# Optimization experiments

Hardware: AMD Instinct MI355X
Metric: run time of the kernel (lower is better)

The kernel has to match this reference:

```python
import jax, jax.numpy as jnp
import numpy as np

WS = 8          # window_size
NH = 8          # num_heads
DIM = 512
EPS = 1e-5


def _layernorm(x, gamma, beta):
    mu = jnp.mean(x, axis=-1, keepdims=True)
    var = jnp.mean(jnp.square(x - mu), axis=-1, keepdims=True)
    return (x - mu) * jax.lax.rsqrt(var + EPS) * gamma + beta


def setup_inputs() -> dict:
    key = jax.random.key(0)
    ks = jax.random.split(key, 16)
    B, C, H, W = 8, DIM, 128, 128
    s = 0.02
    return {
        "x": jax.random.normal(ks[0], (B, C, H, W), jnp.float32),
        "gamma1": jnp.ones((C,), jnp.float32),
        "beta1": jnp.zeros((C,), jnp.float32),
        "gamma2": jnp.ones((C,), jnp.float32),
        "beta2": jnp.zeros((C,), jnp.float32),
        "w_qkv": jax.random.normal(ks[1], (C, 3 * C), jnp.float32) * s,
        "b_qkv": jnp.zeros((3 * C,), jnp.float32),
        "w_out": jax.random.normal(ks[2], (C, C), jnp.float32) * s,
        "b_out": jnp.zeros((C,), jnp.float32),
        "w1": jax.random.normal(ks[3], (C, 4 * C), jnp.float32) * s,
        "b1": jnp.zeros((4 * C,), jnp.float32),
        "w2": jax.random.normal(ks[4], (4 * C, C), jnp.float32) * s,
        "b2": jnp.zeros((C,), jnp.float32),
    }


def reference(x, gamma1, beta1, gamma2, beta2, w_qkv, b_qkv, w_out, b_out, w1, b1, w2, b2):
    B, C, H, W = x.shape
    hd = C // NH          # head_dim = 64
    L = WS * WS           # tokens per window = 64
    N = (H // WS) * (W // WS)

    # window_partition: (B,C,H,W) -> (B,N,C,ws,ws)
    xw = x.reshape(B, C, H // WS, WS, W // WS, WS)
    xw = xw.transpose(0, 1, 2, 4, 3, 5).reshape(B, C, N, WS, WS).transpose(0, 2, 1, 3, 4)
    # spatial_flatten -> (B,N,L,C)
    t = xw.reshape(B, N, C, L).transpose(0, 1, 3, 2)

    # --- attention (non-transposed path) ---
    xn = _layernorm(t, gamma1, beta1)
    qkv = jnp.einsum('bnlc,cd->bnld', xn, w_qkv) + b_qkv
    qkv = qkv.reshape(B, N, L, 3, NH, hd).transpose(3, 0, 1, 4, 2, 5)  # (3,B,N,H,L,hd)
    q, k, v = qkv[0], qkv[1], qkv[2]
    # note: module scales by 1/head_dim on BOTH q and k -> 1/hd^2 total
    scores = jnp.einsum('bnhld,bnhmd->bnhlm', q, k) / (hd * hd)
    attn = jax.nn.softmax(scores, axis=-1)
    o = jnp.einsum('bnhlm,bnhmd->bnhld', attn, v)
    o = o.transpose(0, 1, 3, 2, 4).reshape(B, N, L, C)
    o = jnp.einsum('bnlc,cd->bnld', o, w_out) + b_out
    t = t + o

    # --- MLP ---
    xn2 = _layernorm(t, gamma2, beta2)
    h = jax.nn.gelu(jnp.einsum('bnlc,cd->bnld', xn2, w1) + b1, approximate=False)
    t = t + jnp.einsum('bnld,dc->bnlc', h, w2) + b2

    # spatial_unflatten + window_unpartition -> (B,C,H,W)
    y = t.transpose(0, 1, 3, 2).reshape(B, N, C, WS, WS).transpose(0, 2, 1, 3, 4)
    y = y.reshape(B, C, H // WS, W // WS, WS, WS).transpose(0, 1, 2, 4, 3, 5).reshape(B, C, H, W)
    return y
```

## Files before the change

### kernel.cpp

```cpp
#include <hip/hip_runtime.h>
#include <cstdint>
#include <cstddef>


typedef unsigned short u16;
typedef unsigned int u32;
typedef __attribute__((ext_vector_type(4))) float f32x4;
typedef __attribute__((ext_vector_type(8))) short bf16x8;

#define DEVINL __device__ __forceinline__

DEVINL float bf2f(u16 u){ union { u32 i; float f; } v; v.i = ((u32)u) << 16; return v.f; }
DEVINL u16 f2bf(float f){
  union { float f; u32 i; } v; v.f = f;
  u32 u = v.i;
  u32 r = (u + 0x7fffu + ((u >> 16) & 1u)) >> 16;
  return (u16)r;
}

DEVINL void gload16(u16* lds, const void* g){
  __builtin_amdgcn_global_load_lds(
      (__attribute__((address_space(1))) u32*)(g),
      (__attribute__((address_space(3))) u32*)(lds), 16, 0, 0);
}

__global__ __launch_bounds__(256) void wt_kernel(const float* __restrict__ in,
                                                 u16* __restrict__ out, int K, int N)
{
  __shared__ float tile[64][65];
  int tiles_n = N >> 6;
  int tk = blockIdx.x / tiles_n, tn = blockIdx.x % tiles_n;
  int k0 = tk * 64, n0 = tn * 64;
  int lane = threadIdx.x & 63, wr = threadIdx.x >> 6;
#pragma unroll
  for (int i = 0; i < 16; i++){
    int r = wr * 16 + i;
    tile[r][lane] = in[(size_t)(k0 + r) * N + n0 + lane];
  }
  __syncthreads();
#pragma unroll
  for (int i = 0; i < 16; i++){
    int r = wr * 16 + i;
    out[(size_t)(n0 + r) * K + k0 + lane] = f2bf(tile[lane][r]);
  }
}

template<int MODE>
__global__ __launch_bounds__(256) void ln_kernel(
    const float* __restrict__ x, const u16* __restrict__ o2,
    const float* __restrict__ gamma, const float* __restrict__ beta,
    u16* __restrict__ out)
{
  __shared__ u16 sm[512 * 64];
  int wg = blockIdx.x;
  int b = wg >> 8, n = wg & 255, wy = n >> 4, wx = n & 15;
  int t = threadIdx.x, l = t & 63, wv = t >> 6;
  int yy = l >> 3, xx = l & 7;
  size_t xbase = ((size_t)b * 512) * 16384 + (size_t)(wy * 8 + yy) * 128 + wx * 8 + xx;

#pragma unroll 4
  for (int i = 0; i < 128; i++){
    int c = wv * 128 + i;
    float v = x[xbase + (size_t)c * 16384];
    sm[c * 64 + (l ^ ((2 * (c >> 3)) & 63))] = f2bf(v);
  }
  __syncthreads();

  size_t gbase = (size_t)wg * 64;
  int lane = l;
  int c0 = lane * 8;
  int fs = (2 * lane) & 63;
  float g8[8], b8[8];
#pragma unroll
  for (int j = 0; j < 8; j++){ g8[j] = gamma[c0 + j]; b8[j] = beta[c0 + j]; }

  for (int it = 0; it < 16; it++){
    int tok = wv * 16 + it;
    int lidx = tok ^ fs;
    u16 oarr[8];
    if (MODE == 1){
      uint4 ov = *(const uint4*)&o2[(gbase + tok) * 512 + c0];
      *(uint4*)oarr = ov;
    }
    float tv[8]; float sum = 0.f, sq = 0.f;
#pragma unroll
    for (int j = 0; j < 8; j++){
      float v = bf2f(sm[(c0 + j) * 64 + lidx]);
      if (MODE == 1) v += bf2f(oarr[j]);
      tv[j] = v; sum += v; sq += v * v;
    }
#pragma unroll
    for (int d = 1; d < 64; d <<= 1){
      sum += __shfl_xor(sum, d, 64);
      sq  += __shfl_xor(sq, d, 64);
    }
    float mu = sum * (1.0f / 512.0f);
    float var = sq * (1.0f / 512.0f) - mu * mu;
    float rs = rsqrtf(var + 1e-5f);
    u16 r8[8];
#pragma unroll
    for (int j = 0; j < 8; j++) r8[j] = f2bf((tv[j] - mu) * rs * g8[j] + b8[j]);
    *(uint4*)&out[(gbase + tok) * 512 + c0] = *(uint4*)r8;
  }
}

template<int EPI>
__global__ __launch_bounds__(256) void gemm_kernel(
    const u16* __restrict__ A, const u16* __restrict__ BT,
    const float* __restrict__ bias, const u16* __restrict__ ADD,
    u16* __restrict__ Cout, int N, int K)
{
  __shared__ u16 smem[16384];
  const int nbn = N >> 7;
  int nwg = gridDim.x;
  int bid = blockIdx.x;
  int wgid = (bid & 7) * (nwg >> 3) + (bid >> 3);
  int bm = wgid / nbn, bn = wgid % nbn;
  size_t m0 = (size_t)bm * 128; int n0 = bn * 128;
  int lane = threadIdx.x & 63, wv = threadIdx.x >> 6;
  int wr = wv >> 1, wc = wv & 1;

  f32x4 zero4 = {0.f, 0.f, 0.f, 0.f};
  f32x4 acc[4][4];
#pragma unroll
  for (int i = 0; i < 4; i++)
#pragma unroll
    for (int j = 0; j < 4; j++) acc[i][j] = zero4;

  int srow = wv * 16 + (lane >> 2);
  int scol = (((lane & 3) ^ ((srow >> 1) & 3)) * 8);
  const u16* Abase = A + m0 * (size_t)K;
  const u16* Bbase = BT + (size_t)n0 * K;

  auto STAGE = [&](int buf, int kt){
    u16* as = &smem[buf * 8192];
    u16* bs = as + 4096;
    gload16(as + wv * 512,        Abase + (size_t)srow * K + kt + scol);
    gload16(as + 2048 + wv * 512, Abase + (size_t)(srow + 64) * K + kt + scol);
    gload16(bs + wv * 512,        Bbase + (size_t)srow * K + kt + scol);
    gload16(bs + 2048 + wv * 512, Bbase + (size_t)(srow + 64) * K + kt + scol);
  };

  STAGE(0, 0);
  __syncthreads();

  int nsteps = K >> 5;
  int cur = 0;
  int kslot = lane >> 4;
  for (int t = 0; t < nsteps; ++t){
    if (t + 1 < nsteps) STAGE(cur ^ 1, (t + 1) << 5);
    const u16* as = &smem[cur * 8192];
    const u16* bs = as + 4096;
    bf16x8 af[4], bfr[4];
#pragma unroll
    for (int mt = 0; mt < 4; mt++){
      int row = wr * 64 + mt * 16 + (lane & 15);
      af[mt] = *(const bf16x8*)&as[row * 32 + ((kslot ^ ((row >> 1) & 3)) * 8)];
    }
#pragma unroll
    for (int nt = 0; nt < 4; nt++){
      int row = wc * 64 + nt * 16 + (lane & 15);
      bfr[nt] = *(const bf16x8*)&bs[row * 32 + ((kslot ^ ((row >> 1) & 3)) * 8)];
    }
#pragma unroll
    for (int mt = 0; mt < 4; mt++)
#pragma unroll
      for (int nt = 0; nt < 4; nt++)
        acc[mt][nt] = __builtin_amdgcn_mfma_f32_16x16x32_bf16(af[mt], bfr[nt], acc[mt][nt], 0, 0, 0);
    __syncthreads();
    cur ^= 1;
  }

#pragma unroll
  for (int nt = 0; nt < 4; nt++){
    int cc = wc * 64 + nt * 16 + (lane & 15);
    float bv = bias[n0 + cc];
#pragma unroll
    for (int mt = 0; mt < 4; mt++){
      int r0 = wr * 64 + mt * 16 + ((lane >> 4) * 4);
#pragma unroll
      for (int reg = 0; reg < 4; reg++){
        int rr = r0 + reg;
        float v = acc[mt][nt][reg] + bv;
        if (EPI == 1){
          float h2 = v * v;
          float z = -1.5957691216057308f * (v + 0.044715f * v * h2);
          float e = __expf(z);
          v = v * __builtin_amdgcn_rcpf(1.0f + e);
        }
        smem[rr * 128 + (cc ^ ((rr & 7) << 3))] = f2bf(v);
      }
    }
  }
  __syncthreads();

  int tr = threadIdx.x >> 2;
  int tc = threadIdx.x & 3;
#pragma unroll
  for (int i = 0; i < 2; i++){
    int r = i * 64 + tr;
    size_t gro = (m0 + r) * (size_t)N + n0;
#pragma unroll
    for (int j = 0; j < 4; j++){
      int cw = tc * 8 + j * 32;
      uint4 d = *(const uint4*)&smem[r * 128 + (cw ^ ((r & 7) << 3))];
      if (EPI == 2){
        uint4 av = *(const uint4*)&ADD[gro + cw];
        u16 de[8], ae[8];
        *(uint4*)de = d; *(uint4*)ae = av;
#pragma unroll
        for (int k = 0; k < 8; k++) de[k] = f2bf(bf2f(de[k]) + bf2f(ae[k]));
        d = *(uint4*)de;
      }
      *(uint4*)&Cout[gro + cw] = d;
    }
  }
}

__global__ __launch_bounds__(64) void attn_kernel(const u16* __restrict__ QKV,
                                                  u16* __restrict__ O)
{
  __shared__ u16 qs[4096], ks2[4096], vs[4096], ps[4096];
  int blk = blockIdx.x;
  int wg = blk >> 3, h = blk & 7;
  size_t g0 = (size_t)wg * 64;
  int lane = threadIdx.x;
  int lr = lane >> 3, lch = lane & 7;

#pragma unroll
  for (int it = 0; it < 8; it++){
    int r = it * 8 + lr;
    int sc = lch ^ (r & 7);
    {
      uint4 d = *(const uint4*)&QKV[(g0 + r) * 1536 + h * 64 + lch * 8];
      *(uint4*)&qs[r * 64 + sc * 8] = d;
    }
    {
      uint4 d = *(const uint4*)&QKV[(g0 + r) * 1536 + 512 + h * 64 + lch * 8];
      *(uint4*)&ks2[r * 64 + sc * 8] = d;
    }
    {
      uint4 d = *(const uint4*)&QKV[(g0 + r) * 1536 + 1024 + h * 64 + lch * 8];
      u16 e[8]; *(uint4*)e = d;
      int m = r;
#pragma unroll
      for (int j = 0; j < 8; j++){
        int dd = lch * 8 + j;
        int off = dd * 64 + ((((m * 2) ^ ((dd & 7) << 4))) >> 1);
        vs[off] = e[j];
      }
    }
  }
  __syncthreads();

  f32x4 zero4 = {0.f, 0.f, 0.f, 0.f};
  f32x4 s[4][4];
#pragma unroll
  for (int i = 0; i < 4; i++)
#pragma unroll
    for (int j = 0; j < 4; j++) s[i][j] = zero4;

#pragma unroll
  for (int ks = 0; ks < 2; ks++){
    bf16x8 aq[4], bk[4];
#pragma unroll
    for (int mt = 0; mt < 4; mt++){
      int r = mt * 16 + (lane & 15);
      int cb = (ks * 64 + (lane >> 4) * 16) ^ ((r & 7) << 4);
      aq[mt] = *(const bf16x8*)&qs[r * 64 + (cb >> 1)];
    }
#pragma unroll
    for (int nt = 0; nt < 4; nt++){
      int r = nt * 16 + (lane & 15);
      int cb = (ks * 64 + (lane >> 4) * 16) ^ ((r & 7) << 4);
      bk[nt] = *(const bf16x8*)&ks2[r * 64 + (cb >> 1)];
    }
#pragma unroll
    for (int mt = 0; mt < 4; mt++)
#pragma unroll
      for (int nt = 0; nt < 4; nt++)
        s[mt][nt] = __builtin_amdgcn_mfma_f32_16x16x32_bf16(aq[mt], bk[nt], s[mt][nt], 0, 0, 0);
  }

  const float scl = 1.0f / 4096.0f;
#pragma unroll
  for (int mt = 0; mt < 4; mt++){
#pragma unroll
    for (int reg = 0; reg < 4; reg++){
      float mx = -1e30f;
#pragma unroll
      for (int nt = 0; nt < 4; nt++){
        float v = s[mt][nt][reg] * scl; s[mt][nt][reg] = v; mx = fmaxf(mx, v);
      }
#pragma unroll
      for (int d = 1; d < 16; d <<= 1) mx = fmaxf(mx, __shfl_xor(mx, d, 64));
      float sum = 0.f;
#pragma unroll
      for (int nt = 0; nt < 4; nt++){
        float e = __expf(s[mt][nt][reg] - mx); s[mt][nt][reg] = e; sum += e;
      }
#pragma unroll
      for (int d = 1; d < 16; d <<= 1) sum += __shfl_xor(sum, d, 64);
      float inv = 1.0f / sum;
#pragma unroll
      for (int nt = 0; nt < 4; nt++) s[mt][nt][reg] *= inv;
    }
  }

#pragma unroll
  for (int mt = 0; mt < 4; mt++)
#pragma unroll
    for (int reg = 0; reg < 4; reg++){
      int r = mt * 16 + ((lane >> 4) * 4) + reg;
#pragma unroll
      for (int nt = 0; nt < 4; nt++){
        int c = nt * 16 + (lane & 15);
        ps[r * 64 + ((((c * 2) ^ ((r & 7) << 4))) >> 1)] = f2bf(s[mt][nt][reg]);
      }
    }
  __syncthreads();

  f32x4 o[4][4];
#pragma unroll
  for (int i = 0; i < 4; i++)
#pragma unroll
    for (int j = 0; j < 4; j++) o[i][j] = zero4;

#pragma unroll
  for (int ks = 0; ks < 2; ks++){
    bf16x8 ap[4], bv[4];
#pragma unroll
    for (int mt = 0; mt < 4; mt++){
      int r = mt * 16 + (lane & 15);
      int cb = (ks * 64 + (lane >> 4) * 16) ^ ((r & 7) << 4);
      ap[mt] = *(const bf16x8*)&ps[r * 64 + (cb >> 1)];
    }
#pragma unroll
    for (int nt = 0; nt < 4; nt++){
      int dd = nt * 16 + (lane & 15);
      int cb = (ks * 64 + (lane >> 4) * 16) ^ ((dd & 7) << 4);
      bv[nt] = *(const bf16x8*)&vs[dd * 64 + (cb >> 1)];
    }
#pragma unroll
    for (int mt = 0; mt < 4; mt++)
#pragma unroll
      for (int nt = 0; nt < 4; nt++)
        o[mt][nt] = __builtin_amdgcn_mfma_f32_16x16x32_bf16(ap[mt], bv[nt], o[mt][nt], 0, 0, 0);
  }

#pragma unroll
  for (int mt = 0; mt < 4; mt++)
#pragma unroll
    for (int reg = 0; reg < 4; reg++){
      size_t l = mt * 16 + ((lane >> 4) * 4) + reg;
#pragma unroll
      for (int nt = 0; nt < 4; nt++){
        int dd = nt * 16 + (lane & 15);
        O[(g0 + l) * 512 + h * 64 + dd] = f2bf(o[mt][nt][reg]);
      }
    }
}

__global__ __launch_bounds__(256) void scatter_kernel(
    const float* __restrict__ x, const u16* __restrict__ ms, float* __restrict__ y)
{
  __shared__ u16 sm[512 * 64];
  int wg = blockIdx.x;
  int b = wg >> 8, n = wg & 255, wy = n >> 4, wx = n & 15;
  int t = threadIdx.x, lane = t & 63, wv = t >> 6;
  size_t gbase = (size_t)wg * 64;
  int c0 = lane * 8, fs = (2 * lane) & 63;

  for (int it = 0; it < 16; it++){
    int tok = wv * 16 + it;
    uint4 d = *(const uint4*)&ms[(gbase + tok) * 512 + c0];
    u16 e[8]; *(uint4*)e = d;
    int lidx = tok ^ fs;
#pragma unroll
    for (int j = 0; j < 8; j++) sm[(c0 + j) * 64 + lidx] = e[j];
  }
  __syncthreads();

  int l = lane; int yy = l >> 3, xx = l & 7;
  size_t xbase = ((size_t)b * 512) * 16384 + (size_t)(wy * 8 + yy) * 128 + wx * 8 + xx;
#pragma unroll 4
  for (int i = 0; i < 128; i++){
    int c = wv * 128 + i;
    size_t a = xbase + (size_t)c * 16384;
    y[a] = x[a] + bf2f(sm[c * 64 + (l ^ ((2 * (c >> 3)) & 63))]);
  }
}

extern "C" void kernel_launch(void* const* d_in, const int* in_sizes, int n_in,
                              void* d_out, int out_size, void* d_ws, size_t ws_size,
                              hipStream_t stream)
{
  (void)in_sizes; (void)n_in; (void)out_size; (void)ws_size;
  const float* x      = (const float*)d_in[0];
  const float* gamma1 = (const float*)d_in[1];
  const float* beta1  = (const float*)d_in[2];
  const float* gamma2 = (const float*)d_in[3];
  const float* beta2  = (const float*)d_in[4];
  const float* w_qkv  = (const float*)d_in[5];
  const float* b_qkv  = (const float*)d_in[6];
  const float* w_out  = (const float*)d_in[7];
  const float* b_out  = (const float*)d_in[8];
  const float* w1     = (const float*)d_in[9];
  const float* b1     = (const float*)d_in[10];
  const float* w2     = (const float*)d_in[11];
  const float* b2     = (const float*)d_in[12];
  float* y = (float*)d_out;

  char* ws = (char*)d_ws;
  u16* WqkvT = (u16*)(ws + 0);
  u16* WoutT = (u16*)(ws + 1572864);
  u16* W1T   = (u16*)(ws + 2097152);
  u16* W2T   = (u16*)(ws + 4194304);
  u16* XN    = (u16*)(ws + 6291456);
  u16* O2    = (u16*)(ws + 140509184);
  u16* Obuf  = (u16*)(ws + 274726912);
  u16* QKV   = (u16*)(ws + 408944640);
  u16* Hbuf  = QKV;
  u16* MS    = Obuf;
  const int M = 131072;

  wt_kernel<<<8 * 24, 256, 0, stream>>>(w_qkv, WqkvT, 512, 1536);
  wt_kernel<<<8 * 8,  256, 0, stream>>>(w_out, WoutT, 512, 512);
  wt_kernel<<<8 * 32, 256, 0, stream>>>(w1, W1T, 512, 2048);
  wt_kernel<<<32 * 8, 256, 0, stream>>>(w2, W2T, 2048, 512);

  ln_kernel<0><<<2048, 256, 0, stream>>>(x, nullptr, gamma1, beta1, XN);
  gemm_kernel<0><<<(M / 128) * (1536 / 128), 256, 0, stream>>>(XN, WqkvT, b_qkv, nullptr, QKV, 1536, 512);
  attn_kernel<<<16384, 64, 0, stream>>>(QKV, Obuf);
  gemm_kernel<0><<<(M / 128) * (512 / 128), 256, 0, stream>>>(Obuf, WoutT, b_out, nullptr, O2, 512, 512);
  ln_kernel<1><<<2048, 256, 0, stream>>>(x, O2, gamma2, beta2, XN);
  gemm_kernel<1><<<(M / 128) * (2048 / 128), 256, 0, stream>>>(XN, W1T, b1, nullptr, Hbuf, 2048, 512);
  gemm_kernel<2><<<(M / 128) * (512 / 128), 256, 0, stream>>>(Hbuf, W2T, b2, O2, MS, 512, 2048);
  scatter_kernel<<<2048, 256, 0, stream>>>(x, MS, y);
}
```

Before: 2.457 ms.

## Use 256x256 GEMM tiles with 8 waves and a 4-slot LDS pipeline

Replaces the 128x128, 4-wave GEMM with a 256x256 tile computed by 8 waves. It uses a four-slot LDS ring with three tiles of prefetch and explicit vmcnt waits in place of the double buffer plus __syncthreads, and raises wave priority around the MFMA block. The larger tile raises arithmetic intensity and cuts global traffic per FLOP, while the deeper prefetch hides load latency. In exchange it uses 128KB of LDS and more accumulator registers per block, which limits occupancy. The N=512 GEMMs also launch far fewer blocks, which risks tail imbalance.

```diff
diff --git a/kernel.cpp b/kernel.cpp
--- a/kernel.cpp
+++ b/kernel.cpp
@@ -105,115 +105,115 @@
 }
 
 template<int EPI>
-__global__ __launch_bounds__(256) void gemm_kernel(
+__global__ __launch_bounds__(512, 2) void gemm256_kernel(
     const u16* __restrict__ A, const u16* __restrict__ BT,
     const float* __restrict__ bias, const u16* __restrict__ ADD,
     u16* __restrict__ Cout, int N, int K)
 {
-  __shared__ u16 smem[16384];
-  const int nbn = N >> 7;
+  __shared__ u16 smem[65536];
+  const int nbn = N >> 8;
   int nwg = gridDim.x;
   int bid = blockIdx.x;
   int wgid = (bid & 7) * (nwg >> 3) + (bid >> 3);
   int bm = wgid / nbn, bn = wgid % nbn;
-  size_t m0 = (size_t)bm * 128; int n0 = bn * 128;
-  int lane = threadIdx.x & 63, wv = threadIdx.x >> 6;
-  int wr = wv >> 1, wc = wv & 1;
+  size_t m0 = (size_t)bm * 256; int n0 = bn * 256;
+  int tid = threadIdx.x;
+  int lane = tid & 63, w = tid >> 6;
+  int wr = w >> 2, wc = w & 3;
 
   f32x4 zero4 = {0.f, 0.f, 0.f, 0.f};
-  f32x4 acc[4][4];
-#pragma unroll
-  for (int i = 0; i < 4; i++)
+  f32x4 acc[8][4];
+#pragma unroll
+  for (int i = 0; i < 8; i++)
 #pragma unroll
     for (int j = 0; j < 4; j++) acc[i][j] = zero4;
 
-  int srow = wv * 16 + (lane >> 2);
-  int scol = (((lane & 3) ^ ((srow >> 1) & 3)) * 8);
+  int sr = tid >> 2;
+  int scol = (((tid & 3) ^ ((sr >> 1) & 3)) * 8);
   const u16* Abase = A + m0 * (size_t)K;
   const u16* Bbase = BT + (size_t)n0 * K;
 
-  auto STAGE = [&](int buf, int kt){
-    u16* as = &smem[buf * 8192];
-    u16* bs = as + 4096;
-    gload16(as + wv * 512,        Abase + (size_t)srow * K + kt + scol);
-    gload16(as + 2048 + wv * 512, Abase + (size_t)(srow + 64) * K + kt + scol);
-    gload16(bs + wv * 512,        Bbase + (size_t)srow * K + kt + scol);
-    gload16(bs + 2048 + wv * 512, Bbase + (size_t)(srow + 64) * K + kt + scol);
+  auto STAGE = [&](int slot, int kt){
+    u16* s = &smem[slot * 16384];
+    gload16(s + w * 512,          Abase + (size_t)sr * K + kt + scol);
+    gload16(s + 4096 + w * 512,   Abase + (size_t)(sr + 128) * K + kt + scol);
+    gload16(s + 8192 + w * 512,   Bbase + (size_t)sr * K + kt + scol);
+    gload16(s + 12288 + w * 512,  Bbase + (size_t)(sr + 128) * K + kt + scol);
   };
 
-  STAGE(0, 0);
-  __syncthreads();
-
-  int nsteps = K >> 5;
-  int cur = 0;
+  int nk = K >> 5;
+  STAGE(0, 0); STAGE(1, 32); STAGE(2, 64);
+
   int kslot = lane >> 4;
-  for (int t = 0; t < nsteps; ++t){
-    if (t + 1 < nsteps) STAGE(cur ^ 1, (t + 1) << 5);
-    const u16* as = &smem[cur * 8192];
-    const u16* bs = as + 4096;
-    bf16x8 af[4], bfr[4];
-#pragma unroll
-    for (int mt = 0; mt < 4; mt++){
-      int row = wr * 64 + mt * 16 + (lane & 15);
-      af[mt] = *(const bf16x8*)&as[row * 32 + ((kslot ^ ((row >> 1) & 3)) * 8)];
-    }
-#pragma unroll
-    for (int nt = 0; nt < 4; nt++){
-      int row = wc * 64 + nt * 16 + (lane & 15);
-      bfr[nt] = *(const bf16x8*)&bs[row * 32 + ((kslot ^ ((row >> 1) & 3)) * 8)];
-    }
-#pragma unroll
-    for (int mt = 0; mt < 4; mt++)
-#pragma unroll
-      for (int nt = 0; nt < 4; nt++)
-        acc[mt][nt] = __builtin_amdgcn_mfma_f32_16x16x32_bf16(af[mt], bfr[nt], acc[mt][nt], 0, 0, 0);
-    __syncthreads();
-    cur ^= 1;
-  }
-
-#pragma unroll
-  for (int nt = 0; nt < 4; nt++){
-    int cc = wc * 64 + nt * 16 + (lane & 15);
+  for (int t = 0; t < nk; ++t){
+    if (t < nk - 2)      asm volatile("s_waitcnt vmcnt(8)" ::: "memory");
+    else if (t == nk - 2) asm volatile("s_waitcnt vmcnt(4)" ::: "memory");
+    else                  asm volatile("s_waitcnt vmcnt(0)" ::: "memory");
+    __builtin_amdgcn_s_barrier();
+    if (t + 3 < nk) STAGE((t + 3) & 3, (t + 3) << 5);
+
+    const u16* as = &smem[(t & 3) * 16384];
+    const u16* bs = as + 8192;
+    bf16x8 af[8], bf[4];
+#pragma unroll
+    for (int m = 0; m < 8; m++){
+      int row = wr * 128 + m * 16 + (lane & 15);
+      af[m] = *(const bf16x8*)&as[row * 32 + ((kslot ^ ((row >> 1) & 3)) * 8)];
+    }
+#pragma unroll
+    for (int n = 0; n < 4; n++){
+      int row = wc * 64 + n * 16 + (lane & 15);
+      bf[n] = *(const bf16x8*)&bs[row * 32 + ((kslot ^ ((row >> 1) & 3)) * 8)];
+    }
+    __builtin_amdgcn_s_setprio(1);
+#pragma unroll
+    for (int m = 0; m < 8; m++)
+#pragma unroll
+      for (int n = 0; n < 4; n++)
+        acc[m][n] = __builtin_amdgcn_mfma_f32_16x16x32_bf16(af[m], bf[n], acc[m][n], 0, 0, 0);
+    __builtin_amdgcn_s_setprio(0);
+  }
+
+  __syncthreads();
+
+#pragma unroll
+  for (int n = 0; n < 4; n++){
+    int cc = wc * 64 + n * 16 + (lane & 15);
     float bv = bias[n0 + cc];
 #pragma unroll
-    for (int mt = 0; mt < 4; mt++){
-      int r0 = wr * 64 + mt * 16 + ((lane >> 4) * 4);
+    for (int m = 0; m < 8; m++){
+      int r0 = wr * 128 + m * 16 + ((lane >> 4) * 4);
 #pragma unroll
       for (int reg = 0; reg < 4; reg++){
         int rr = r0 + reg;
-        float v = acc[mt][nt][reg] + bv;
+        float v = acc[m][n][reg] + bv;
         if (EPI == 1){
           float h2 = v * v;
           float z = -1.5957691216057308f * (v + 0.044715f * v * h2);
           float e = __expf(z);
           v = v * __builtin_amdgcn_rcpf(1.0f + e);
         }
-        smem[rr * 128 + (cc ^ ((rr & 7) << 3))] = f2bf(v);
-      }
-    }
-  }
-  __syncthreads();
-
-  int tr = threadIdx.x >> 2;
-  int tc = threadIdx.x & 3;
-#pragma unroll
-  for (int i = 0; i < 2; i++){
-    int r = i * 64 + tr;
-    size_t gro = (m0 + r) * (size_t)N + n0;
-#pragma unroll
-    for (int j = 0; j < 4; j++){
-      int cw = tc * 8 + j * 32;
-      uint4 d = *(const uint4*)&smem[r * 128 + (cw ^ ((r & 7) << 3))];
-      if (EPI == 2){
-        uint4 av = *(const uint4*)&ADD[gro + cw];
-        u16 de[8], ae[8];
-        *(uint4*)de = d; *(uint4*)ae = av;
-#pragma unroll
-        for (int k = 0; k < 8; k++) de[k] = f2bf(bf2f(de[k]) + bf2f(ae[k]));
-        d = *(uint4*)de;
-      }
-      *(uint4*)&Cout[gro + cw] = d;
-    }
+        smem[rr * 256 + (cc ^ ((rr & 31) << 3))] = f2bf(v);
+      }
+    }
+  }
+  __syncthreads();
+
+#pragma unroll
+  for (int i = 0; i < 16; i++){
+    int c = i * 512 + tid;
+    int row = c >> 5, g = c & 31;
+    size_t gro = (m0 + row) * (size_t)N + n0 + g * 8;
+    uint4 d = *(const uint4*)&smem[row * 256 + ((g ^ (row & 31)) << 3)];
+    if (EPI == 2){
+      uint4 av = *(const uint4*)&ADD[gro];
+      u16 de[8], ae[8];
+      *(uint4*)de = d; *(uint4*)ae = av;
+#pragma unroll
+      for (int k = 0; k < 8; k++) de[k] = f2bf(bf2f(de[k]) + bf2f(ae[k]));
+      d = *(uint4*)de;
+    }
+    *(uint4*)&Cout[gro] = d;
   }
 }
 
@@ -430,11 +430,11 @@
   wt_kernel<<<32 * 8, 256, 0, stream>>>(w2, W2T, 2048, 512);
 
   ln_kernel<0><<<2048, 256, 0, stream>>>(x, nullptr, gamma1, beta1, XN);
-  gemm_kernel<0><<<(M / 128) * (1536 / 128), 256, 0, stream>>>(XN, WqkvT, b_qkv, nullptr, QKV, 1536, 512);
+  gemm256_kernel<0><<<(M / 256) * (1536 / 256), 512, 0, stream>>>(XN, WqkvT, b_qkv, nullptr, QKV, 1536, 512);
   attn_kernel<<<16384, 64, 0, stream>>>(QKV, Obuf);
-  gemm_kernel<0><<<(M / 128) * (512 / 128), 256, 0, stream>>>(Obuf, WoutT, b_out, nullptr, O2, 512, 512);
+  gemm256_kernel<0><<<(M / 256) * (512 / 256), 512, 0, stream>>>(Obuf, WoutT, b_out, nullptr, O2, 512, 512);
   ln_kernel<1><<<2048, 256, 0, stream>>>(x, O2, gamma2, beta2, XN);
-  gemm_kernel<1><<<(M / 128) * (2048 / 128), 256, 0, stream>>>(XN, W1T, b1, nullptr, Hbuf, 2048, 512);
-  gemm_kernel<2><<<(M / 128) * (512 / 128), 256, 0, stream>>>(Hbuf, W2T, b2, O2, MS, 512, 2048);
+  gemm256_kernel<1><<<(M / 256) * (2048 / 256), 512, 0, stream>>>(XN, W1T, b1, nullptr, Hbuf, 2048, 512);
+  gemm256_kernel<2><<<(M / 256) * (512 / 256), 512, 0, stream>>>(Hbuf, W2T, b2, O2, MS, 512, 2048);
   scatter_kernel<<<2048, 256, 0, stream>>>(x, MS, y);
 }
```

Measured after the change: 2.362 ms. 3.9% less time.
